# Performance work log

Measured on AMD Instinct MI355X. Metric: run time of the kernel, lower is better.

Reference implementation:

```python
import jax, jax.numpy as jnp
import numpy as np

N, E, D, H, Z, HEADS = 20000, 160000, 3000, 512, 50, 3
EPS = 1e-5


def _bn(x, gamma, beta):
    # BatchNorm1d, training-mode stats (biased variance), eps=1e-5
    m = x.mean(axis=0)
    v = x.var(axis=0)
    return (x - m) * jax.lax.rsqrt(v + EPS) * gamma + beta


def _gat(x, src, dst, n, W, att_src, att_dst, bias, heads, c):
    # PyG GATConv, concat=False (mean over heads), negative_slope=0.2
    h = (x @ W).reshape(n, heads, c)                      # [N,H,C]
    a_s = (h * att_src).sum(-1)                           # [N,H]
    a_d = (h * att_dst).sum(-1)                           # [N,H]
    e = jax.nn.leaky_relu(a_s[src] + a_d[dst], 0.2)       # [Etot,H]
    e = e - jax.ops.segment_max(e, dst, num_segments=n)[dst]
    ex = jnp.exp(e)
    den = jax.ops.segment_sum(ex, dst, num_segments=n)[dst]
    alpha = ex / den                                      # segment softmax over incoming edges
    msg = h[src] * alpha[:, :, None]                      # [Etot,H,C]
    out = jax.ops.segment_sum(msg, dst, num_segments=n)   # [N,H,C]
    return out.mean(axis=1) + bias


def setup_inputs() -> dict:
    key = jax.random.key(0)
    ks = jax.random.split(key, 16)
    s = 0.05
    inp = {
        "x": jax.random.normal(ks[0], (N, D), dtype=jnp.float32),
        "edge_index": jax.random.randint(ks[1], (2, E), 0, N, dtype=jnp.int64),
        "W1": jax.random.normal(ks[2], (D, HEADS * H), dtype=jnp.float32) * s,
        "att_src1": jax.random.normal(ks[3], (HEADS, H), dtype=jnp.float32) * s,
        "att_dst1": jax.random.normal(ks[4], (HEADS, H), dtype=jnp.float32) * s,
        "b1": jnp.zeros((H,), jnp.float32),
        "bn1_g": jnp.ones((H,), jnp.float32),
        "bn1_b": jnp.zeros((H,), jnp.float32),
        "W2": jax.random.normal(ks[5], (H, HEADS * Z), dtype=jnp.float32) * s,
        "att_src2": jax.random.normal(ks[6], (HEADS, Z), dtype=jnp.float32) * s,
        "att_dst2": jax.random.normal(ks[7], (HEADS, Z), dtype=jnp.float32) * s,
        "b2": jnp.zeros((Z,), jnp.float32),
        "bn2_g": jnp.ones((Z,), jnp.float32),
        "bn2_b": jnp.zeros((Z,), jnp.float32),
        "lin1_w": jax.random.normal(ks[8], (H, Z), dtype=jnp.float32) * s,
        "lin1_b": jnp.zeros((H,), jnp.float32),
        "dbn_g": jnp.ones((H,), jnp.float32),
        "dbn_b": jnp.zeros((H,), jnp.float32),
        "lin2_w": jax.random.normal(ks[9], (D, H), dtype=jnp.float32) * s,
        "lin2_b": jnp.zeros((D,), jnp.float32),
    }
    return inp


def reference(x, edge_index, W1, att_src1, att_dst1, b1, bn1_g, bn1_b,
              W2, att_src2, att_dst2, b2, bn2_g, bn2_b,
              lin1_w, lin1_b, dbn_g, dbn_b, lin2_w, lin2_b):
    n = x.shape[0]
    loop = jnp.arange(n, dtype=edge_index.dtype)
    src = jnp.concatenate([edge_index[0], loop])  # add self-loops (PyG default)
    dst = jnp.concatenate([edge_index[1], loop])
    h = jax.nn.relu(_bn(_gat(x, src, dst, n, W1, att_src1, att_dst1, b1, HEADS, H), bn1_g, bn1_b))
    z = jax.nn.relu(_bn(_gat(h, src, dst, n, W2, att_src2, att_dst2, b2, HEADS, Z), bn2_g, bn2_b))
    d = jax.nn.relu(_bn(z @ lin1_w.T + lin1_b, dbn_g, dbn_b))
    out = jax.nn.relu(d @ lin2_w.T + lin2_b)
    return out
```

## Files before the change

### kernel.cpp

```cpp
#include <hip/hip_runtime.h>
#include <stdint.h>

typedef unsigned short u16;
typedef __attribute__((ext_vector_type(8))) short s16x8;
typedef __attribute__((ext_vector_type(4))) short s16x4;
typedef __attribute__((ext_vector_type(4))) float f32x4;

#define DEVFN static __device__ __forceinline__

static constexpr int NN = 20000;
static constexpr int EE = 160000;
static constexpr int ET = 180000;
static constexpr int DD = 3000;
static constexpr int HH = 512;
static constexpr int ZZ = 50;
static constexpr int C1 = 1536;
static constexpr int C2 = 150;
static constexpr int KP1 = 3008;

DEVFN u16 f2b(float f) {
  uint32_t u = __builtin_bit_cast(uint32_t, f);
  u += 0x7FFFu + ((u >> 16) & 1u);
  return (u16)(u >> 16);
}
DEVFN float b2f(u16 b) {
  uint32_t u = ((uint32_t)b) << 16;
  return __builtin_bit_cast(float, u);
}
DEVFN int edge_at(const void* ei, int mode32, long idx) {
  return mode32 ? ((const int*)ei)[idx] : (int)((const long long*)ei)[idx];
}

typedef __attribute__((address_space(1))) const unsigned int gas_uint;
typedef __attribute__((address_space(3))) unsigned int las_uint;
DEVFN void async16(const u16* g, u16* l) {
  __builtin_amdgcn_global_load_lds((gas_uint*)(uintptr_t)g,
                                   (las_uint*)(unsigned)(uintptr_t)l, 16, 0, 0);
}

__global__ void k_detect(const int* __restrict__ ei, int* __restrict__ mode) {
  __shared__ int nz;
  if (threadIdx.x == 0) nz = 0;
  __syncthreads();
  int loc = 0;
  for (int i = threadIdx.x; i < 1024; i += blockDim.x)
    if (ei[2 * i + 1] != 0) loc = 1;
  if (loc) atomicOr(&nz, 1);
  __syncthreads();
  if (threadIdx.x == 0) *mode = nz;
}

__global__ void k_deg(const void* ei, const int* __restrict__ mode, int* __restrict__ deg) {
  int m = *mode;
  long i = (long)blockIdx.x * blockDim.x + threadIdx.x;
  long st = (long)gridDim.x * blockDim.x;
  for (; i < ET; i += st) {
    int d = (i < EE) ? edge_at(ei, m, EE + i) : (int)(i - EE);
    if ((unsigned)d < (unsigned)NN) atomicAdd(&deg[d], 1);
  }
}

__global__ void k_scan_blk(const int* __restrict__ deg, int* __restrict__ rowptr,
                           int* __restrict__ bsum) {
  __shared__ int buf[256];
  int b = blockIdx.x, tid = threadIdx.x;
  int i = b * 256 + tid;
  buf[tid] = (i < NN) ? deg[i] : 0;
  __syncthreads();
  for (int off = 1; off < 256; off <<= 1) {
    int t = (tid >= off) ? buf[tid - off] : 0;
    __syncthreads();
    buf[tid] += t;
    __syncthreads();
  }
  if (i < NN) rowptr[i + 1] = buf[tid];
  if (tid == 255) bsum[b] = buf[255];
}
__global__ void k_scan_top(int* __restrict__ bsum, int nb) {
  __shared__ int buf[128];
  int tid = threadIdx.x;
  buf[tid] = (tid < nb) ? bsum[tid] : 0;
  __syncthreads();
  for (int off = 1; off < 128; off <<= 1) {
    int t = (tid >= off) ? buf[tid - off] : 0;
    __syncthreads();
    buf[tid] += t;
    __syncthreads();
  }
  if (tid < nb) bsum[tid] = buf[tid];
}
__global__ void k_scan_add(int* __restrict__ rowptr, const int* __restrict__ bsum) {
  int b = blockIdx.x, tid = threadIdx.x;
  int i = b * 256 + tid;
  if (i == 0) rowptr[0] = 0;
  if (b > 0 && i < NN) rowptr[i + 1] += bsum[b - 1];
}

__global__ void k_fill(const void* ei, const int* __restrict__ mode,
                       const int* __restrict__ rowptr, int* __restrict__ cursor,
                       int* __restrict__ srcp) {
  int m = *mode;
  long i = (long)blockIdx.x * blockDim.x + threadIdx.x;
  long st = (long)gridDim.x * blockDim.x;
  for (; i < ET; i += st) {
    int s, d;
    if (i < EE) { s = edge_at(ei, m, i); d = edge_at(ei, m, EE + i); }
    else { s = d = (int)(i - EE); }
    if ((unsigned)d < (unsigned)NN && (unsigned)s < (unsigned)NN) {
      int pos = atomicAdd(&cursor[d], 1);
      srcp[rowptr[d] + pos] = s;
    }
  }
}

__global__ void k_cvt_pad4(const float* __restrict__ in, u16* __restrict__ out,
                           int R, int Cin, int ldo) {
  int r = blockIdx.y;
  int c = (blockIdx.x * blockDim.x + threadIdx.x) * 4;
  if (c >= ldo) return;
  s16x4 o;
  const float* src = in + (size_t)r * Cin + c;
  if (r < R && c + 4 <= Cin && ((((size_t)r * Cin + c) & 3) == 0)) {
    f32x4 v = *(const f32x4*)src;
#pragma unroll
    for (int j = 0; j < 4; j++) o[j] = (short)f2b(v[j]);
  } else {
#pragma unroll
    for (int j = 0; j < 4; j++)
      o[j] = (short)((r < R && c + j < Cin) ? f2b(src[j]) : (u16)0);
  }
  *(s16x4*)(out + (size_t)r * ldo + c) = o;
}

__global__ void k_transpose_tile(const float* __restrict__ in, u16* __restrict__ out,
                                 int R, int Cc, int ldo) {
  __shared__ float t[32][33];
  int tx = threadIdx.x & 31, ty = threadIdx.x >> 5;
  int c0 = blockIdx.x * 32, r0 = blockIdx.y * 32;
#pragma unroll
  for (int j = 0; j < 4; j++) {
    int r = r0 + ty + j * 8, c = c0 + tx;
    t[ty + j * 8][tx] = (r < R && c < Cc) ? in[(size_t)r * Cc + c] : 0.f;
  }
  __syncthreads();
#pragma unroll
  for (int j = 0; j < 4; j++) {
    int c = c0 + ty + j * 8, r = r0 + tx;
    if (c < Cc && r < ldo) out[(size_t)c * ldo + r] = f2b(t[tx][ty + j * 8]);
  }
}

__global__ void k_transpose_cvt2(const float* __restrict__ in, u16* __restrict__ out,
                                 int R, int C, int Cp, int ldo) {
  long total = (long)Cp * ldo;
  long i = (long)blockIdx.x * blockDim.x + threadIdx.x;
  long st = (long)gridDim.x * blockDim.x;
  for (; i < total; i += st) {
    int c = (int)(i / ldo), r = (int)(i % ldo);
    out[i] = (c < C && r < R) ? f2b(in[(size_t)r * C + c]) : (u16)0;
  }
}

template<bool OUT_BF16, bool RELU>
__global__ __launch_bounds__(256) void k_gemm3(
    const u16* __restrict__ Ag, const u16* __restrict__ Bg, void* __restrict__ Cg,
    const float* __restrict__ bias, int M, int Nn, int Kp, int ld, int ldc) {
  __shared__ __align__(16) u16 As[2][128][64];
  __shared__ __align__(16) u16 Bs[2][128][64];
  int tid = threadIdx.x;
  int lane = tid & 63, wid = tid >> 6;
  int wm = wid >> 1, wn = wid & 1;
  int lr = lane & 15, lg = lane >> 4;
  int m0 = blockIdx.y * 128, n0 = blockIdx.x * 128;

  int srow = lane >> 3;
  int skk = ((lane & 7) ^ srow) * 8;
  const u16* agp[4];
  const u16* bgp[4];
#pragma unroll
  for (int i = 0; i < 4; i++) {
    int ra = wid * 32 + i * 8 + srow;
    int ga = m0 + ra; if (ga > M - 1) ga = M - 1;
    agp[i] = Ag + (size_t)ga * ld + skk;
    bgp[i] = Bg + (size_t)(n0 + ra) * ld + skk;
  }

#define STAGE(bufi, kofs) do {                                   \
    u16* la_ = &As[bufi][0][0] + wid * 2048;                     \
    u16* lb_ = &Bs[bufi][0][0] + wid * 2048;                     \
    _Pragma("unroll")                                            \
    for (int i_ = 0; i_ < 4; i_++) {                             \
      async16(agp[i_] + (kofs), la_ + i_ * 512);                 \
      async16(bgp[i_] + (kofs), lb_ + i_ * 512);                 \
    }                                                            \
  } while (0)

  f32x4 acc[4][4];
#pragma unroll
  for (int mi = 0; mi < 4; mi++)
#pragma unroll
    for (int ni = 0; ni < 4; ni++) {
      acc[mi][ni][0] = 0.f; acc[mi][ni][1] = 0.f; acc[mi][ni][2] = 0.f; acc[mi][ni][3] = 0.f;
    }

  int rx = lr & 7;
  int NT = Kp >> 6;
  STAGE(0, 0);
  for (int t = 0; t < NT; t++) {
    int cur = t & 1;
    if (t + 1 < NT) {
      STAGE(cur ^ 1, (t + 1) * 64);
      asm volatile("s_waitcnt vmcnt(8)" ::: "memory");
    } else {
      asm volatile("s_waitcnt vmcnt(0)" ::: "memory");
    }
    __builtin_amdgcn_s_barrier();
    asm volatile("" ::: "memory");
#pragma unroll
    for (int ks = 0; ks < 2; ks++) {
      int ch = ((ks * 4 + lg) ^ rx) * 8;
      s16x8 a[4], b[4];
#pragma unroll
      for (int mi = 0; mi < 4; mi++)
        a[mi] = *(const s16x8*)&As[cur][wm * 64 + mi * 16 + lr][ch];
#pragma unroll
      for (int ni = 0; ni < 4; ni++)
        b[ni] = *(const s16x8*)&Bs[cur][wn * 64 + ni * 16 + lr][ch];
#pragma unroll
      for (int mi = 0; mi < 4; mi++)
#pragma unroll
        for (int ni = 0; ni < 4; ni++)
          acc[mi][ni] = __builtin_amdgcn_mfma_f32_16x16x32_bf16(a[mi], b[ni], acc[mi][ni], 0, 0, 0);
    }
    asm volatile("" ::: "memory");
    __builtin_amdgcn_s_barrier();
  }
#undef STAGE

#pragma unroll
  for (int mi = 0; mi < 4; mi++)
#pragma unroll
    for (int ni = 0; ni < 4; ni++) {
      int col = n0 + wn * 64 + ni * 16 + lr;
      if (col >= Nn) continue;
      float bv = bias ? bias[col] : 0.f;
#pragma unroll
      for (int j = 0; j < 4; j++) {
        int row = m0 + wm * 64 + mi * 16 + lg * 4 + j;
        if (row >= M) continue;
        float v = acc[mi][ni][j] + bv;
        if (RELU) v = v > 0.f ? v : 0.f;
        if (OUT_BF16) ((u16*)Cg)[(size_t)row * ldc + col] = f2b(v);
        else          ((float*)Cg)[(size_t)row * ldc + col] = v;
      }
    }
}

__global__ void k_attdot1b(const u16* __restrict__ h1b, const float* __restrict__ asrc,
                           const float* __restrict__ adst, float* __restrict__ as_,
                           float* __restrict__ ad_) {
  int n = blockIdx.x;
  int hd = threadIdx.x >> 6, lane = threadIdx.x & 63;
  s16x8 h = *(const s16x8*)(h1b + (size_t)n * C1 + hd * 512 + lane * 8);
  const float* ap = asrc + hd * 512 + lane * 8;
  const float* dp = adst + hd * 512 + lane * 8;
  f32x4 a0 = *(const f32x4*)ap, a1 = *(const f32x4*)(ap + 4);
  f32x4 d0 = *(const f32x4*)dp, d1 = *(const f32x4*)(dp + 4);
  float ps = 0.f, pd = 0.f;
#pragma unroll
  for (int j = 0; j < 4; j++) {
    float hv = b2f((u16)h[j]);
    ps += hv * a0[j]; pd += hv * d0[j];
    float hw = b2f((u16)h[j + 4]);
    ps += hw * a1[j]; pd += hw * d1[j];
  }
  for (int off = 32; off; off >>= 1) { ps += __shfl_xor(ps, off); pd += __shfl_xor(pd, off); }
  if (lane == 0) { as_[3 * n + hd] = ps; ad_[3 * n + hd] = pd; }
}

__global__ void k_attdot2(const float* __restrict__ s2, const float* __restrict__ asrc,
                          const float* __restrict__ adst, float* __restrict__ as_,
                          float* __restrict__ ad_) {
  int n = blockIdx.x, tid = threadIdx.x;
  for (int hd = 0; hd < 3; hd++) {
    float ps = 0.f, pd = 0.f;
    if (tid < 50) {
      float v = s2[(size_t)n * C2 + hd * 50 + tid];
      ps = v * asrc[hd * 50 + tid];
      pd = v * adst[hd * 50 + tid];
    }
    for (int off = 32; off; off >>= 1) { ps += __shfl_xor(ps, off); pd += __shfl_xor(pd, off); }
    if (tid == 0) { as_[3 * n + hd] = ps; ad_[3 * n + hd] = pd; }
  }
}

__global__ void k_gat1(const u16* __restrict__ h1b, const float* __restrict__ as1,
                       const float* __restrict__ ad1, const int* __restrict__ rowptr,
                       const int* __restrict__ srcp, const float* __restrict__ bias,
                       float* __restrict__ out) {
  int n = blockIdx.x, tid = threadIdx.x;
  __shared__ float sm[3], sden[3];
  __shared__ int s_src[128];
  __shared__ float s_alpha[128][3];
  int r0 = rowptr[n], deg = rowptr[n + 1] - r0;
  float adl[3] = {ad1[3 * n], ad1[3 * n + 1], ad1[3 * n + 2]};

  if (tid < 64) {
    float mx[3] = {-1e30f, -1e30f, -1e30f};
    for (int e = tid; e < deg; e += 64) {
      int s = srcp[r0 + e];
#pragma unroll
      for (int hd = 0; hd < 3; hd++) {
        float v = as1[3 * s + hd] + adl[hd];
        v = v > 0.f ? v : 0.2f * v;
        mx[hd] = fmaxf(mx[hd], v);
      }
    }
#pragma unroll
    for (int hd = 0; hd < 3; hd++)
      for (int off = 32; off; off >>= 1) mx[hd] = fmaxf(mx[hd], __shfl_xor(mx[hd], off));
    float sd[3] = {0.f, 0.f, 0.f};
    for (int e = tid; e < deg; e += 64) {
      int s = srcp[r0 + e];
#pragma unroll
      for (int hd = 0; hd < 3; hd++) {
        float v = as1[3 * s + hd] + adl[hd];
        v = v > 0.f ? v : 0.2f * v;
        sd[hd] += __expf(v - mx[hd]);
      }
    }
#pragma unroll
    for (int hd = 0; hd < 3; hd++)
      for (int off = 32; off; off >>= 1) sd[hd] += __shfl_xor(sd[hd], off);
    if (tid == 0) {
#pragma unroll
      for (int hd = 0; hd < 3; hd++) { sm[hd] = mx[hd]; sden[hd] = sd[hd]; }
    }
  }
  __syncthreads();

  float a0 = 0.f, a1 = 0.f;
  for (int base = 0; base < deg; base += 128) {
    int cnt = min(128, deg - base);
    if (tid < cnt) {
      int s = srcp[r0 + base + tid];
      s_src[tid] = s;
#pragma unroll
      for (int hd = 0; hd < 3; hd++) {
        float v = as1[3 * s + hd] + adl[hd];
        v = v > 0.f ? v : 0.2f * v;
        s_alpha[tid][hd] = __expf(v - sm[hd]) / sden[hd];
      }
    }
    __syncthreads();
    int e = 0;
    for (; e + 2 <= cnt; e += 2) {
      const u16* h0 = h1b + (size_t)s_src[e] * C1 + 2 * tid;
      const u16* h1 = h1b + (size_t)s_src[e + 1] * C1 + 2 * tid;
      uint32_t u0[3], u1[3];
#pragma unroll
      for (int hd = 0; hd < 3; hd++) {
        u0[hd] = *(const uint32_t*)(h0 + hd * 512);
        u1[hd] = *(const uint32_t*)(h1 + hd * 512);
      }
#pragma unroll
      for (int hd = 0; hd < 3; hd++) {
        float al0 = s_alpha[e][hd], al1 = s_alpha[e + 1][hd];
        a0 += al0 * b2f((u16)u0[hd]) + al1 * b2f((u16)u1[hd]);
        a1 += al0 * b2f((u16)(u0[hd] >> 16)) + al1 * b2f((u16)(u1[hd] >> 16));
      }
    }
    if (e < cnt) {
      const u16* h0 = h1b + (size_t)s_src[e] * C1 + 2 * tid;
#pragma unroll
      for (int hd = 0; hd < 3; hd++) {
        uint32_t u = *(const uint32_t*)(h0 + hd * 512);
        float al = s_alpha[e][hd];
        a0 += al * b2f((u16)u);
        a1 += al * b2f((u16)(u >> 16));
      }
    }
    __syncthreads();
  }
  float2 bv = *(const float2*)(bias + 2 * tid);
  float2 ov = {a0 * (1.f / 3.f) + bv.x, a1 * (1.f / 3.f) + bv.y};
  *(float2*)(out + (size_t)n * 512 + 2 * tid) = ov;
}

__global__ void k_gat2(const float* __restrict__ s2, const float* __restrict__ as2,
                       const float* __restrict__ ad2, const int* __restrict__ rowptr,
                       const int* __restrict__ srcp, const float* __restrict__ bias,
                       float* __restrict__ z) {
  int n = blockIdx.x, tid = threadIdx.x;
  __shared__ int s_src[64];
  __shared__ float s_alpha[64][3];
  int r0 = rowptr[n], deg = rowptr[n + 1] - r0;
  float adl[3] = {ad2[3 * n], ad2[3 * n + 1], ad2[3 * n + 2]};

  float mx[3] = {-1e30f, -1e30f, -1e30f};
  for (int e = tid; e < deg; e += 64) {
    int s = srcp[r0 + e];
#pragma unroll
    for (int hd = 0; hd < 3; hd++) {
      float v = as2[3 * s + hd] + adl[hd];
      v = v > 0.f ? v : 0.2f * v;
      mx[hd] = fmaxf(mx[hd], v);
    }
  }
#pragma unroll
  for (int hd = 0; hd < 3; hd++)
    for (int off = 32; off; off >>= 1) mx[hd] = fmaxf(mx[hd], __shfl_xor(mx[hd], off));
  float sd[3] = {0.f, 0.f, 0.f};
  for (int e = tid; e < deg; e += 64) {
    int s = srcp[r0 + e];
#pragma unroll
    for (int hd = 0; hd < 3; hd++) {
      float v = as2[3 * s + hd] + adl[hd];
      v = v > 0.f ? v : 0.2f * v;
      sd[hd] += __expf(v - mx[hd]);
    }
  }
#pragma unroll
  for (int hd = 0; hd < 3; hd++)
    for (int off = 32; off; off >>= 1) sd[hd] += __shfl_xor(sd[hd], off);

  float acc = 0.f;
  for (int base = 0; base < deg; base += 64) {
    int cnt = min(64, deg - base);
    if (tid < cnt) {
      int s = srcp[r0 + base + tid];
      s_src[tid] = s;
#pragma unroll
      for (int hd = 0; hd < 3; hd++) {
        float v = as2[3 * s + hd] + adl[hd];
        v = v > 0.f ? v : 0.2f * v;
        s_alpha[tid][hd] = __expf(v - mx[hd]) / sd[hd];
      }
    }
    __syncthreads();
    if (tid < 50) {
      for (int e = 0; e < cnt; e++) {
        const float* row = s2 + (size_t)s_src[e] * C2;
#pragma unroll
        for (int hd = 0; hd < 3; hd++) acc += s_alpha[e][hd] * row[hd * 50 + tid];
      }
    }
    __syncthreads();
  }
  if (tid < 50) z[(size_t)n * ZZ + tid] = acc * (1.f / 3.f) + bias[tid];
}

__global__ void k_colstats3(const float* __restrict__ x, float* __restrict__ gsum,
                            float* __restrict__ gsq, long total, int C) {
  long i = (long)blockIdx.x * blockDim.x + threadIdx.x;
  long st = (long)gridDim.x * blockDim.x;
  int c = (int)(i % C);
  float s = 0.f, q = 0.f;
  for (; i < total; i += st) { float v = x[i]; s += v; q += v * v; }
  atomicAdd(&gsum[c], s);
  atomicAdd(&gsq[c], q);
}

__global__ void k_bnfinal(const float* __restrict__ gsum, const float* __restrict__ gsq,
                          const float* __restrict__ g, const float* __restrict__ b,
                          float* __restrict__ scale, float* __restrict__ shift,
                          int C, float invN) {
  int c = blockIdx.x * blockDim.x + threadIdx.x;
  if (c < C) {
    float m = gsum[c] * invN;
    float var = gsq[c] * invN - m * m;
    float rs = rsqrtf(var + 1e-5f);
    float sc = g[c] * rs;
    scale[c] = sc;
    shift[c] = b[c] - m * sc;
  }
}

__global__ void k_bnrelu4(const float* __restrict__ x, const float* __restrict__ sc,
                          const float* __restrict__ sh, u16* __restrict__ out, long total4) {
  long i = (long)blockIdx.x * blockDim.x + threadIdx.x;
  long st = (long)gridDim.x * blockDim.x;
  for (; i < total4; i += st) {
    long b = i * 4;
    int c = (int)(b & 511);
    f32x4 v = *(const f32x4*)(x + b);
    f32x4 s = *(const f32x4*)(sc + c);
    f32x4 t = *(const f32x4*)(sh + c);
    s16x4 o;
#pragma unroll
    for (int j = 0; j < 4; j++) {
      float r = v[j] * s[j] + t[j];
      r = r > 0.f ? r : 0.f;
      o[j] = (short)f2b(r);
    }
    *(s16x4*)(out + b) = o;
  }
}

template<int C, int LDO>
__global__ void k_bnrelu(const float* __restrict__ x, const float* __restrict__ scale,
                         const float* __restrict__ shift, u16* __restrict__ out, long total) {
  long i = (long)blockIdx.x * blockDim.x + threadIdx.x;
  long st = (long)gridDim.x * blockDim.x;
  for (; i < total; i += st) {
    int c = (int)(i % C);
    long r = i / C;
    float v = x[i] * scale[c] + shift[c];
    v = v > 0.f ? v : 0.f;
    out[r * LDO + c] = f2b(v);
  }
}

extern "C" void kernel_launch(void* const* d_in, const int* in_sizes, int n_in,
                              void* d_out, int out_size, void* d_ws, size_t ws_size,
                              hipStream_t stream) {
  (void)in_sizes; (void)n_in; (void)out_size;
  const float* x     = (const float*)d_in[0];
  const void*  ei    = d_in[1];
  const float* W1    = (const float*)d_in[2];
  const float* asrc1 = (const float*)d_in[3];
  const float* adst1 = (const float*)d_in[4];
  const float* b1    = (const float*)d_in[5];
  const float* bn1g  = (const float*)d_in[6];
  const float* bn1b  = (const float*)d_in[7];
  const float* W2    = (const float*)d_in[8];
  const float* asrc2 = (const float*)d_in[9];
  const float* adst2 = (const float*)d_in[10];
  const float* b2    = (const float*)d_in[11];
  const float* bn2g  = (const float*)d_in[12];
  const float* bn2b  = (const float*)d_in[13];
  const float* l1w   = (const float*)d_in[14];
  const float* l1b   = (const float*)d_in[15];
  const float* dbng  = (const float*)d_in[16];
  const float* dbnb  = (const float*)d_in[17];
  const float* l2w   = (const float*)d_in[18];
  const float* l2b   = (const float*)d_in[19];
  float* out = (float*)d_out;
  char* ws = (char*)d_ws;

  size_t off = 0;
  auto alloc = [&](size_t b) { size_t r = off; off += (b + 255) & ~(size_t)255; return r; };
  const size_t oXB  = alloc(120320000);
  const size_t oH1  = alloc(61440000);
  const size_t oW1T = alloc((size_t)C1 * KP1 * 2);
  const size_t oAS1 = alloc((size_t)NN * 12), oAD1 = alloc((size_t)NN * 12);
  const size_t oAS2 = alloc((size_t)NN * 12), oAD2 = alloc((size_t)NN * 12);
  const size_t oRP  = alloc((size_t)(NN + 1) * 4);
  const size_t oDEG = alloc((size_t)NN * 4);
  const size_t oSRC = alloc((size_t)ET * 4);
  const size_t oMODE = alloc(256);
  const size_t oBSUM = alloc(512);
  const size_t oSUM = alloc(2048), oSQ = alloc(2048);
  const size_t oSC = alloc(2048), oSH = alloc(2048);
  if (ws_size < off) return;

  u16*   xb   = (u16*)(ws + oXB);
  float* g1   = (float*)(ws + oXB);
  u16*   h2b  = (u16*)(ws + oXB + 40960000);
  float* s2   = (float*)(ws + oXB + 61440000);
  float* zf   = (float*)(ws + oXB + 73440000);
  u16*   zb   = (u16*)(ws + oXB + 77440000);
  u16*   w2T  = (u16*)(ws + oXB + 80000000);
  u16*   l1wT = (u16*)(ws + oXB + 80262400);
  u16*   l2wT = (u16*)(ws + oXB + 80328192);
  float* dbuf = (float*)(ws + oXB);
  u16*   h1b  = (u16*)(ws + oH1);
  u16*   db   = (u16*)(ws + oH1);
  u16*   w1T  = (u16*)(ws + oW1T);
  int* mode   = (int*)(ws + oMODE);
  int* bsum   = (int*)(ws + oBSUM);
  int* deg    = (int*)(ws + oDEG);
  int* rowptr = (int*)(ws + oRP);
  int* srcp   = (int*)(ws + oSRC);
  float *as1 = (float*)(ws + oAS1), *ad1 = (float*)(ws + oAD1);
  float *as2 = (float*)(ws + oAS2), *ad2 = (float*)(ws + oAD2);
  float *gsum = (float*)(ws + oSUM), *gsq = (float*)(ws + oSQ);
  float *bsc = (float*)(ws + oSC), *bsh = (float*)(ws + oSH);

  k_detect<<<1, 256, 0, stream>>>((const int*)ei, mode);
  hipMemsetAsync(deg, 0, (size_t)NN * 4, stream);
  k_deg<<<512, 256, 0, stream>>>(ei, mode, deg);
  k_scan_blk<<<79, 256, 0, stream>>>(deg, rowptr, bsum);
  k_scan_top<<<1, 128, 0, stream>>>(bsum, 79);
  k_scan_add<<<79, 256, 0, stream>>>(rowptr, bsum);
  hipMemsetAsync(deg, 0, (size_t)NN * 4, stream);
  k_fill<<<512, 256, 0, stream>>>(ei, mode, rowptr, deg, srcp);

  k_cvt_pad4<<<dim3(3, NN), 256, 0, stream>>>(x, xb, NN, DD, KP1);
  k_transpose_tile<<<dim3(C1 / 32, KP1 / 32), 256, 0, stream>>>(W1, w1T, DD, C1, KP1);
  k_gemm3<true, false><<<dim3(12, 157), 256, 0, stream>>>(xb, w1T, h1b, nullptr,
                                                          NN, C1, KP1, KP1, C1);
  k_attdot1b<<<NN, 192, 0, stream>>>(h1b, asrc1, adst1, as1, ad1);
  k_gat1<<<NN, 256, 0, stream>>>(h1b, as1, ad1, rowptr, srcp, b1, g1);
  hipMemsetAsync(gsum, 0, 2048, stream);
  hipMemsetAsync(gsq, 0, 2048, stream);
  k_colstats3<<<512, 256, 0, stream>>>(g1, gsum, gsq, (long)NN * HH, HH);
  k_bnfinal<<<2, 256, 0, stream>>>(gsum, gsq, bn1g, bn1b, bsc, bsh, HH, 1.0f / NN);
  k_bnrelu4<<<2048, 256, 0, stream>>>(g1, bsc, bsh, h2b, (long)NN * HH / 4);

  k_transpose_cvt2<<<256, 256, 0, stream>>>(W2, w2T, HH, C2, 256, HH);
  k_gemm3<false, false><<<dim3(2, 157), 256, 0, stream>>>(h2b, w2T, s2, nullptr,
                                                          NN, C2, HH, HH, C2);
  k_attdot2<<<NN, 64, 0, stream>>>(s2, asrc2, adst2, as2, ad2);
  k_gat2<<<NN, 64, 0, stream>>>(s2, as2, ad2, rowptr, srcp, b2, zf);
  hipMemsetAsync(gsum, 0, 2048, stream);
  hipMemsetAsync(gsq, 0, 2048, stream);
  k_colstats3<<<25, 256, 0, stream>>>(zf, gsum, gsq, (long)NN * ZZ, ZZ);
  k_bnfinal<<<1, 64, 0, stream>>>(gsum, gsq, bn2g, bn2b, bsc, bsh, ZZ, 1.0f / NN);
  hipMemsetAsync(zb, 0, (size_t)NN * 64 * 2, stream);
  k_bnrelu<50, 64><<<512, 256, 0, stream>>>(zf, bsc, bsh, zb, (long)NN * ZZ);

  k_cvt_pad4<<<dim3(1, HH), 256, 0, stream>>>(l1w, l1wT, HH, ZZ, 64);
  k_gemm3<false, false><<<dim3(4, 157), 256, 0, stream>>>(zb, l1wT, dbuf, l1b,
                                                          NN, HH, 64, 64, HH);
  hipMemsetAsync(gsum, 0, 2048, stream);
  hipMemsetAsync(gsq, 0, 2048, stream);
  k_colstats3<<<512, 256, 0, stream>>>(dbuf, gsum, gsq, (long)NN * HH, HH);
  k_bnfinal<<<2, 256, 0, stream>>>(gsum, gsq, dbng, dbnb, bsc, bsh, HH, 1.0f / NN);
  k_bnrelu4<<<2048, 256, 0, stream>>>(dbuf, bsc, bsh, db, (long)NN * HH / 4);
  k_cvt_pad4<<<dim3(1, 3072), 256, 0, stream>>>(l2w, l2wT, DD, HH, HH);
  k_gemm3<false, true><<<dim3(24, 157), 256, 0, stream>>>(db, l2wT, out, l2b,
                                                          NN, DD, HH, HH, DD);
}
```

Baseline: 818.3 us.

## Swizzle GEMM tiles per XCD, vectorize GAT1 gather, fold memsets into kernels

The GEMM maps workgroup IDs so that consecutive tiles land on the same XCD, which should improve L2 reuse on the chiplet layout. k_gat1 now uses 192 threads, one wave per head, with 16-byte vector gathers and a cross-head reduction in shared memory, replacing the 4-byte loads. The hipMemsetAsync calls for the BN statistic buffers are removed by giving each BN its own buffers and zeroing them inside the attdot kernels. The pre-zeroing memset of zb is replaced by a padded BN-ReLU kernel that writes the zeros itself. The in-kernel zeroing only works because block 0 of an earlier kernel finishes before the colstats launch in stream order.

Result: no change. 807.7 us (-1.3%).

```diff
diff --git a/kernel.cpp b/kernel.cpp
--- a/kernel.cpp
+++ b/kernel.cpp
@@ -171,7 +171,13 @@
   int lane = tid & 63, wid = tid >> 6;
   int wm = wid >> 1, wn = wid & 1;
   int lr = lane & 15, lg = lane >> 4;
-  int m0 = blockIdx.y * 128, n0 = blockIdx.x * 128;
+
+  int nwg = gridDim.x * gridDim.y;
+  int wg = blockIdx.y * gridDim.x + blockIdx.x;
+  int q = nwg >> 3, r = nwg & 7;
+  int xcd = wg & 7, loc = wg >> 3;
+  int swz = (xcd < r ? xcd * (q + 1) : r * (q + 1) + (xcd - r) * q) + loc;
+  int m0 = (swz / gridDim.x) * 128, n0 = (swz % gridDim.x) * 128;
 
   int srow = lane >> 3;
   int skk = ((lane & 7) ^ srow) * 8;
@@ -258,8 +264,12 @@
 
 __global__ void k_attdot1b(const u16* __restrict__ h1b, const float* __restrict__ asrc,
                            const float* __restrict__ adst, float* __restrict__ as_,
-                           float* __restrict__ ad_) {
+                           float* __restrict__ ad_, float* __restrict__ z0,
+                           float* __restrict__ z1) {
   int n = blockIdx.x;
+  if (n == 0) {
+    for (int i = threadIdx.x; i < HH; i += 192) { z0[i] = 0.f; z1[i] = 0.f; }
+  }
   int hd = threadIdx.x >> 6, lane = threadIdx.x & 63;
   s16x8 h = *(const s16x8*)(h1b + (size_t)n * C1 + hd * 512 + lane * 8);
   const float* ap = asrc + hd * 512 + lane * 8;
@@ -280,8 +290,14 @@
 
 __global__ void k_attdot2(const float* __restrict__ s2, const float* __restrict__ asrc,
                           const float* __restrict__ adst, float* __restrict__ as_,
-                          float* __restrict__ ad_) {
+                          float* __restrict__ ad_, float* __restrict__ z0,
+                          float* __restrict__ z1, float* __restrict__ z2,
+                          float* __restrict__ z3) {
   int n = blockIdx.x, tid = threadIdx.x;
+  if (n == 0) {
+    for (int i = tid; i < HH; i += 64) { z2[i] = 0.f; z3[i] = 0.f; }
+    if (tid < 50) { z0[tid] = 0.f; z1[tid] = 0.f; }
+  }
   for (int hd = 0; hd < 3; hd++) {
     float ps = 0.f, pd = 0.f;
     if (tid < 50) {
@@ -294,14 +310,16 @@
   }
 }
 
-__global__ void k_gat1(const u16* __restrict__ h1b, const float* __restrict__ as1,
-                       const float* __restrict__ ad1, const int* __restrict__ rowptr,
-                       const int* __restrict__ srcp, const float* __restrict__ bias,
-                       float* __restrict__ out) {
+__global__ __launch_bounds__(192) void k_gat1(
+    const u16* __restrict__ h1b, const float* __restrict__ as1,
+    const float* __restrict__ ad1, const int* __restrict__ rowptr,
+    const int* __restrict__ srcp, const float* __restrict__ bias,
+    float* __restrict__ out) {
   int n = blockIdx.x, tid = threadIdx.x;
   __shared__ float sm[3], sden[3];
   __shared__ int s_src[128];
   __shared__ float s_alpha[128][3];
+  __shared__ float part[3][512];
   int r0 = rowptr[n], deg = rowptr[n + 1] - r0;
   float adl[3] = {ad1[3 * n], ad1[3 * n + 1], ad1[3 * n + 2]};
 
@@ -339,52 +357,58 @@
   }
   __syncthreads();
 
-  float a0 = 0.f, a1 = 0.f;
+  int hd = tid >> 6, lane = tid & 63;
+  float a[8];
+#pragma unroll
+  for (int j = 0; j < 8; j++) a[j] = 0.f;
+
   for (int base = 0; base < deg; base += 128) {
     int cnt = min(128, deg - base);
     if (tid < cnt) {
       int s = srcp[r0 + base + tid];
       s_src[tid] = s;
 #pragma unroll
-      for (int hd = 0; hd < 3; hd++) {
-        float v = as1[3 * s + hd] + adl[hd];
+      for (int h2 = 0; h2 < 3; h2++) {
+        float v = as1[3 * s + h2] + adl[h2];
         v = v > 0.f ? v : 0.2f * v;
-        s_alpha[tid][hd] = __expf(v - sm[hd]) / sden[hd];
+        s_alpha[tid][h2] = __expf(v - sm[h2]) / sden[h2];
       }
     }
     __syncthreads();
     int e = 0;
     for (; e + 2 <= cnt; e += 2) {
-      const u16* h0 = h1b + (size_t)s_src[e] * C1 + 2 * tid;
-      const u16* h1 = h1b + (size_t)s_src[e + 1] * C1 + 2 * tid;
-      uint32_t u0[3], u1[3];
-#pragma unroll
-      for (int hd = 0; hd < 3; hd++) {
-        u0[hd] = *(const uint32_t*)(h0 + hd * 512);
-        u1[hd] = *(const uint32_t*)(h1 + hd * 512);
-      }
-#pragma unroll
-      for (int hd = 0; hd < 3; hd++) {
-        float al0 = s_alpha[e][hd], al1 = s_alpha[e + 1][hd];
-        a0 += al0 * b2f((u16)u0[hd]) + al1 * b2f((u16)u1[hd]);
-        a1 += al0 * b2f((u16)(u0[hd] >> 16)) + al1 * b2f((u16)(u1[hd] >> 16));
-      }
+      const u16* p0 = h1b + (size_t)s_src[e] * C1 + (hd << 9) + lane * 8;
+      const u16* p1 = h1b + (size_t)s_src[e + 1] * C1 + (hd << 9) + lane * 8;
+      s16x8 v0 = *(const s16x8*)p0;
+      s16x8 v1 = *(const s16x8*)p1;
+      float al0 = s_alpha[e][hd], al1 = s_alpha[e + 1][hd];
+#pragma unroll
+      for (int j = 0; j < 8; j++)
+        a[j] += al0 * b2f((u16)v0[j]) + al1 * b2f((u16)v1[j]);
     }
     if (e < cnt) {
-      const u16* h0 = h1b + (size_t)s_src[e] * C1 + 2 * tid;
-#pragma unroll
-      for (int hd = 0; hd < 3; hd++) {
-        uint32_t u = *(const uint32_t*)(h0 + hd * 512);
-        float al = s_alpha[e][hd];
-        a0 += al * b2f((u16)u);
-        a1 += al * b2f((u16)(u >> 16));
-      }
-    }
-    __syncthreads();
-  }
-  float2 bv = *(const float2*)(bias + 2 * tid);
-  float2 ov = {a0 * (1.f / 3.f) + bv.x, a1 * (1.f / 3.f) + bv.y};
-  *(float2*)(out + (size_t)n * 512 + 2 * tid) = ov;
+      const u16* p0 = h1b + (size_t)s_src[e] * C1 + (hd << 9) + lane * 8;
+      s16x8 v0 = *(const s16x8*)p0;
+      float al0 = s_alpha[e][hd];
+#pragma unroll
+      for (int j = 0; j < 8; j++) a[j] += al0 * b2f((u16)v0[j]);
+    }
+    __syncthreads();
+  }
+
+#pragma unroll
+  for (int j = 0; j < 8; j++) part[hd][lane * 8 + j] = a[j];
+  __syncthreads();
+  if (tid < 128) {
+    f32x4 p0 = *(const f32x4*)&part[0][tid * 4];
+    f32x4 p1 = *(const f32x4*)&part[1][tid * 4];
+    f32x4 p2 = *(const f32x4*)&part[2][tid * 4];
+    f32x4 bv = *(const f32x4*)(bias + tid * 4);
+    f32x4 o;
+#pragma unroll
+    for (int j = 0; j < 4; j++) o[j] = (p0[j] + p1[j] + p2[j]) * (1.f / 3.f) + bv[j];
+    *(f32x4*)(out + (size_t)n * 512 + tid * 4) = o;
+  }
 }
 
 __global__ void k_gat2(const float* __restrict__ s2, const float* __restrict__ as2,
@@ -497,18 +521,17 @@
   }
 }
 
-template<int C, int LDO>
-__global__ void k_bnrelu(const float* __restrict__ x, const float* __restrict__ scale,
-                         const float* __restrict__ shift, u16* __restrict__ out, long total) {
-  long i = (long)blockIdx.x * blockDim.x + threadIdx.x;
-  long st = (long)gridDim.x * blockDim.x;
-  for (; i < total; i += st) {
-    int c = (int)(i % C);
-    long r = i / C;
-    float v = x[i] * scale[c] + shift[c];
+__global__ void k_bnrelu_pad(const float* __restrict__ x, const float* __restrict__ sc,
+                             const float* __restrict__ sh, u16* __restrict__ out) {
+  int i = blockIdx.x * blockDim.x + threadIdx.x;
+  if (i >= NN * 64) return;
+  int c = i & 63, r = i >> 6;
+  float v = 0.f;
+  if (c < 50) {
+    v = x[r * 50 + c] * sc[c] + sh[c];
     v = v > 0.f ? v : 0.f;
-    out[r * LDO + c] = f2b(v);
-  }
+  }
+  out[i] = f2b(v);
 }
 
 extern "C" void kernel_launch(void* const* d_in, const int* in_sizes, int n_in,
@@ -550,7 +573,9 @@
   const size_t oSRC = alloc((size_t)ET * 4);
   const size_t oMODE = alloc(256);
   const size_t oBSUM = alloc(512);
-  const size_t oSUM = alloc(2048), oSQ = alloc(2048);
+  const size_t oS1 = alloc(2048), oQ1 = alloc(2048);
+  const size_t oS2 = alloc(2048), oQ2 = alloc(2048);
+  const size_t oS3 = alloc(2048), oQ3 = alloc(2048);
   const size_t oSC = alloc(2048), oSH = alloc(2048);
   if (ws_size < off) return;
 
@@ -574,7 +599,9 @@
   int* srcp   = (int*)(ws + oSRC);
   float *as1 = (float*)(ws + oAS1), *ad1 = (float*)(ws + oAD1);
   float *as2 = (float*)(ws + oAS2), *ad2 = (float*)(ws + oAD2);
-  float *gsum = (float*)(ws + oSUM), *gsq = (float*)(ws + oSQ);
+  float *sum1 = (float*)(ws + oS1), *sq1 = (float*)(ws + oQ1);
+  float *sum2 = (float*)(ws + oS2), *sq2 = (float*)(ws + oQ2);
+  float *sum3 = (float*)(ws + oS3), *sq3 = (float*)(ws + oQ3);
   float *bsc = (float*)(ws + oSC), *bsh = (float*)(ws + oSH);
 
   k_detect<<<1, 256, 0, stream>>>((const int*)ei, mode);
@@ -590,33 +617,26 @@
   k_transpose_tile<<<dim3(C1 / 32, KP1 / 32), 256, 0, stream>>>(W1, w1T, DD, C1, KP1);
   k_gemm3<true, false><<<dim3(12, 157), 256, 0, stream>>>(xb, w1T, h1b, nullptr,
                                                           NN, C1, KP1, KP1, C1);
-  k_attdot1b<<<NN, 192, 0, stream>>>(h1b, asrc1, adst1, as1, ad1);
-  k_gat1<<<NN, 256, 0, stream>>>(h1b, as1, ad1, rowptr, srcp, b1, g1);
-  hipMemsetAsync(gsum, 0, 2048, stream);
-  hipMemsetAsync(gsq, 0, 2048, stream);
-  k_colstats3<<<512, 256, 0, stream>>>(g1, gsum, gsq, (long)NN * HH, HH);
-  k_bnfinal<<<2, 256, 0, stream>>>(gsum, gsq, bn1g, bn1b, bsc, bsh, HH, 1.0f / NN);
+  k_attdot1b<<<NN, 192, 0, stream>>>(h1b, asrc1, adst1, as1, ad1, sum1, sq1);
+  k_gat1<<<NN, 192, 0, stream>>>(h1b, as1, ad1, rowptr, srcp, b1, g1);
+  k_colstats3<<<512, 256, 0, stream>>>(g1, sum1, sq1, (long)NN * HH, HH);
+  k_bnfinal<<<2, 256, 0, stream>>>(sum1, sq1, bn1g, bn1b, bsc, bsh, HH, 1.0f / NN);
   k_bnrelu4<<<2048, 256, 0, stream>>>(g1, bsc, bsh, h2b, (long)NN * HH / 4);
 
   k_transpose_cvt2<<<256, 256, 0, stream>>>(W2, w2T, HH, C2, 256, HH);
   k_gemm3<false, false><<<dim3(2, 157), 256, 0, stream>>>(h2b, w2T, s2, nullptr,
                                                           NN, C2, HH, HH, C2);
-  k_attdot2<<<NN, 64, 0, stream>>>(s2, asrc2, adst2, as2, ad2);
+  k_attdot2<<<NN, 64, 0, stream>>>(s2, asrc2, adst2, as2, ad2, sum2, sq2, sum3, sq3);
   k_gat2<<<NN, 64, 0, stream>>>(s2, as2, ad2, rowptr, srcp, b2, zf);
-  hipMemsetAsync(gsum, 0, 2048, stream);
-  hipMemsetAsync(gsq, 0, 2048, stream);
-  k_colstats3<<<25, 256, 0, stream>>>(zf, gsum, gsq, (long)NN * ZZ, ZZ);
-  k_bnfinal<<<1, 64, 0, stream>>>(gsum, gsq, bn2g, bn2b, bsc, bsh, ZZ, 1.0f / NN);
-  hipMemsetAsync(zb, 0, (size_t)NN * 64 * 2, stream);
-  k_bnrelu<50, 64><<<512, 256, 0, stream>>>(zf, bsc, bsh, zb, (long)NN * ZZ);
+  k_colstats3<<<25, 256, 0, stream>>>(zf, sum2, sq2, (long)NN * ZZ, ZZ);
+  k_bnfinal<<<1, 64, 0, stream>>>(sum2, sq2, bn2g, bn2b, bsc, bsh, ZZ, 1.0f / NN);
+  k_bnrelu_pad<<<5000, 256, 0, stream>>>(zf, bsc, bsh, zb);
 
   k_cvt_pad4<<<dim3(1, HH), 256, 0, stream>>>(l1w, l1wT, HH, ZZ, 64);
   k_gemm3<false, false><<<dim3(4, 157), 256, 0, stream>>>(zb, l1wT, dbuf, l1b,
                                                           NN, HH, 64, 64, HH);
-  hipMemsetAsync(gsum, 0, 2048, stream);
-  hipMemsetAsync(gsq, 0, 2048, stream);
-  k_colstats3<<<512, 256, 0, stream>>>(dbuf, gsum, gsq, (long)NN * HH, HH);
-  k_bnfinal<<<2, 256, 0, stream>>>(gsum, gsq, dbng, dbnb, bsc, bsh, HH, 1.0f / NN);
+  k_colstats3<<<512, 256, 0, stream>>>(dbuf, sum3, sq3, (long)NN * HH, HH);
+  k_bnfinal<<<2, 256, 0, stream>>>(sum3, sq3, dbng, dbnb, bsc, bsh, HH, 1.0f / NN);
   k_bnrelu4<<<2048, 256, 0, stream>>>(dbuf, bsc, bsh, db, (long)NN * HH / 4);
   k_cvt_pad4<<<dim3(1, 3072), 256, 0, stream>>>(l2w, l2wT, DD, HH, HH);
   k_gemm3<false, true><<<dim3(24, 157), 256, 0, stream>>>(db, l2wT, out, l2b,
```
